# Kernel tuning notes

Measured on AMD Instinct MI355X. Metric: run time of the kernel, lower is better.

## Reference

```python
import jax, jax.numpy as jnp
import numpy as np

NC = 6  # number of classes (model=None default)
BOX_GAIN, CLS_GAIN, DFL_GAIN = 7.5, 0.5, 1.5


def setup_inputs() -> dict:
    key = jax.random.key(0)
    k0, k1, k2, kb, kc, kxy, kwh = jax.random.split(key, 7)
    bs, na, no = 32, 3, NC + 5
    pred0 = jax.random.normal(k0, (bs, na, 160, 160, no), dtype=jnp.float32)
    pred1 = jax.random.normal(k1, (bs, na, 80, 80, no), dtype=jnp.float32)
    pred2 = jax.random.normal(k2, (bs, na, 40, 40, no), dtype=jnp.float32)
    n_tgt = 8192
    b = jax.random.randint(kb, (n_tgt,), 0, bs).astype(jnp.float32)
    c = jax.random.randint(kc, (n_tgt,), 0, NC).astype(jnp.float32)
    xy = jax.random.uniform(kxy, (n_tgt, 2), minval=0.02, maxval=0.98)
    wh = jax.random.uniform(kwh, (n_tgt, 2), minval=0.02, maxval=0.3)
    targets = jnp.concatenate([b[:, None], c[:, None], xy, wh], axis=1)  # [N,6]
    return {"pred0": pred0, "pred1": pred1, "pred2": pred2, "targets": targets}


def _layer_loss(pred, b, c, txywh):
    # pred: [bs, na, ny, nx, no]; matches: per-target gather at anchor 0
    bs, na, ny, nx, no = pred.shape
    n = txywh.shape[0]
    # int(nx*tx) truncation; coords positive so floor == trunc
    gx = jnp.clip(jnp.floor(nx * txywh[:, 0]).astype(jnp.int32), 0, nx - 1)
    gy = jnp.clip(jnp.floor(ny * txywh[:, 1]).astype(jnp.int32), 0, ny - 1)
    p = pred[b, 0, gy, gx]  # [N, no] gathered predictions
    lbox = jnp.abs(p[:, :4] - txywh).sum()                 # L1, reduction='sum'
    lobj = jax.nn.softplus(-p[:, 4]).sum()                 # BCE-with-logits vs 1
    p_cls = p[:, 5:5 + NC]                                  # [N, NC]
    t_cls = jax.nn.one_hot(c, NC, dtype=p_cls.dtype)
    lcls = (jax.nn.softplus(p_cls) - p_cls * t_cls).sum()  # BCE-with-logits vs one-hot
    inv_n = 1.0 / jnp.maximum(1, n)
    return lbox * inv_n, lobj * inv_n, lcls * inv_n


def reference(pred0, pred1, pred2, targets):
    b = targets[:, 0].astype(jnp.int32)
    c = targets[:, 1].astype(jnp.int32)
    txywh = targets[:, 2:6]
    lbox = jnp.zeros((), jnp.float32)
    lobj = jnp.zeros((), jnp.float32)
    lcls = jnp.zeros((), jnp.float32)
    for pred in (pred0, pred1, pred2):
        db, do, dc = _layer_loss(pred, b, c, txywh)
        lbox, lobj, lcls = lbox + db, lobj + do, lcls + dc
    # NOTE: source multiplies lobj by dfl_gain (reproduced faithfully)
    lbox = lbox * BOX_GAIN
    lobj = lobj * DFL_GAIN
    lcls = lcls * CLS_GAIN
    loss = lbox + lobj + lcls
    return loss, lbox, lobj, lcls
```

## Files before the change

kernel.cpp:

```cpp
#include <hip/hip_runtime.h>

#define NCLS 6
#define NO 11
#define TAG 0x5D3C0DEu

__device__ __forceinline__ float softplusf(float x) {
    return log1pf(expf(-fabsf(x))) + fmaxf(x, 0.0f);
}

__global__ void __launch_bounds__(256) detloss_fused(
        const float* __restrict__ pred0,
        const float* __restrict__ pred1,
        const float* __restrict__ pred2,
        const float* __restrict__ targets,
        unsigned long long* __restrict__ slots,
        float* __restrict__ out,
        int n_tgt, int nwaves, float inv_n) {
    const int stride = gridDim.x * blockDim.x;
    float lbox = 0.0f, lobj = 0.0f, lcls = 0.0f;
    for (int i = blockIdx.x * blockDim.x + threadIdx.x; i < n_tgt; i += stride) {
        const float2* t2 = (const float2*)(targets + (size_t)i * 6);
        const float2 q0 = t2[0], q1 = t2[1], q2 = t2[2];
        const int   b  = (int)q0.x;
        const int   c  = (int)q0.y;
        const float tx = q1.x, ty = q1.y, tw = q2.x, th = q2.y;
        const float* preds[3] = {pred0, pred1, pred2};
        const int    dims[3]  = {160, 80, 40};
        #pragma unroll
        for (int l = 0; l < 3; ++l) {
            const int nx = dims[l], ny = dims[l];
            int gx = (int)floorf((float)nx * tx); gx = min(max(gx, 0), nx - 1);
            int gy = (int)floorf((float)ny * ty); gy = min(max(gy, 0), ny - 1);
            const float* p = preds[l] +
                ((size_t)b * 3u * (size_t)ny * (size_t)nx +
                 (size_t)gy * (size_t)nx + (size_t)gx) * NO;
            lbox += fabsf(p[0] - tx) + fabsf(p[1] - ty) +
                    fabsf(p[2] - tw) + fabsf(p[3] - th);
            lobj += softplusf(-p[4]);
            float prod = 1.0f;
            #pragma unroll
            for (int j = 0; j < NCLS; ++j) prod *= (1.0f + expf(p[5 + j]));
            lcls += logf(prod) - p[5 + c];
        }
    }

    #pragma unroll
    for (int off = 32; off > 0; off >>= 1) {
        lbox += __shfl_down(lbox, off);
        lobj += __shfl_down(lobj, off);
        lcls += __shfl_down(lcls, off);
    }
    const int wid  = threadIdx.x >> 6;
    const int lane = threadIdx.x & 63;
    const int wglobal = blockIdx.x * (blockDim.x >> 6) + wid;
    if (lane == 0) {
        const int s0 = wglobal * 3;
        atomicExch(&slots[s0 + 0], ((unsigned long long)TAG << 32) | __float_as_uint(lbox));
        atomicExch(&slots[s0 + 1], ((unsigned long long)TAG << 32) | __float_as_uint(lobj));
        atomicExch(&slots[s0 + 2], ((unsigned long long)TAG << 32) | __float_as_uint(lcls));
    }
    if (blockIdx.x != 0) return;

    __shared__ float sP[3][128];
    __shared__ float sR[3];
    const int tid    = threadIdx.x;
    const int nslots = nwaves * 3;
    if (tid < nslots) {
        unsigned long long w;
        do { w = atomicAdd(&slots[tid], 0ull); } while ((unsigned)(w >> 32) != TAG);
        atomicExch(&slots[tid], 0ull);
        sP[tid % 3][tid / 3] = __uint_as_float((unsigned)w);
    }
    if (tid + 256 < nslots) {
        const int s = tid + 256;
        unsigned long long w;
        do { w = atomicAdd(&slots[s], 0ull); } while ((unsigned)(w >> 32) != TAG);
        atomicExch(&slots[s], 0ull);
        sP[s % 3][s / 3] = __uint_as_float((unsigned)w);
    }
    __syncthreads();

    if (wid < 3) {
        float v = sP[wid][lane] + sP[wid][lane + 64];
        #pragma unroll
        for (int off = 32; off > 0; off >>= 1) v += __shfl_down(v, off);
        if (lane == 0) sR[wid] = v;
    }
    __syncthreads();

    if (tid == 0) {
        const float LB = sR[0] * inv_n * 7.5f;
        const float LO = sR[1] * inv_n * 1.5f;
        const float LC = sR[2] * inv_n * 0.5f;
        out[0] = LB + LO + LC;
        out[1] = LB;
        out[2] = LO;
        out[3] = LC;
    }
}

extern "C" void kernel_launch(void* const* d_in, const int* in_sizes, int n_in,
                              void* d_out, int out_size, void* d_ws, size_t ws_size,
                              hipStream_t stream) {
    const float* pred0   = (const float*)d_in[0];
    const float* pred1   = (const float*)d_in[1];
    const float* pred2   = (const float*)d_in[2];
    const float* targets = (const float*)d_in[3];
    float* out = (float*)d_out;
    unsigned long long* slots = (unsigned long long*)d_ws;

    const int n_tgt = in_sizes[3] / 6;
    const float inv_n = 1.0f / (float)(n_tgt > 0 ? n_tgt : 1);

    const int block = 256;
    int grid = (n_tgt + block - 1) / block;
    if (grid > 32) grid = 32;
    const int nwaves = grid * (block / 64);

    detloss_fused<<<grid, block, 0, stream>>>(pred0, pred1, pred2, targets,
                                              slots, out, n_tgt, nwaves, inv_n);
}
```

Measured before the change: 9.974 us.

## Dedicate block zero to reduction and replace RMW atomics with relaxed loads/stores

Adds a separate consumer block that only gathers the per-wave partial sums, so the producer blocks no longer include one that also spins. Replaces atomicAdd-polling and atomicExch with relaxed agent-scope atomic loads and stores. Folds the per-target softplus and log calls into running products with a single log at the end, which removes transcendental work but risks overflow or underflow of the product over many targets per thread.

```diff
diff --git a/kernel.cpp b/kernel.cpp
--- a/kernel.cpp
+++ b/kernel.cpp
@@ -3,10 +3,6 @@
 #define NCLS 6
 #define NO 11
 #define TAG 0x5D3C0DEu
-
-__device__ __forceinline__ float softplusf(float x) {
-    return log1pf(expf(-fabsf(x))) + fmaxf(x, 0.0f);
-}
 
 __global__ void __launch_bounds__(256) detloss_fused(
         const float* __restrict__ pred0,
@@ -16,69 +12,88 @@
         unsigned long long* __restrict__ slots,
         float* __restrict__ out,
         int n_tgt, int nwaves, float inv_n) {
-    const int stride = gridDim.x * blockDim.x;
-    float lbox = 0.0f, lobj = 0.0f, lcls = 0.0f;
-    for (int i = blockIdx.x * blockDim.x + threadIdx.x; i < n_tgt; i += stride) {
-        const float2* t2 = (const float2*)(targets + (size_t)i * 6);
-        const float2 q0 = t2[0], q1 = t2[1], q2 = t2[2];
-        const int   b  = (int)q0.x;
-        const int   c  = (int)q0.y;
-        const float tx = q1.x, ty = q1.y, tw = q2.x, th = q2.y;
-        const float* preds[3] = {pred0, pred1, pred2};
-        const int    dims[3]  = {160, 80, 40};
+    const int tid  = threadIdx.x;
+    const int wid  = tid >> 6;
+    const int lane = tid & 63;
+
+    if (blockIdx.x != 0) {
+        const int nprod  = gridDim.x - 1;
+        const int stride = nprod * blockDim.x;
+        float lbox = 0.0f, prod_obj = 1.0f, prod_cls = 1.0f, sub = 0.0f;
+        for (int i = (blockIdx.x - 1) * blockDim.x + tid; i < n_tgt; i += stride) {
+            const float2* t2 = (const float2*)(targets + (size_t)i * 6);
+            const float2 q0 = t2[0], q1 = t2[1], q2 = t2[2];
+            const int   b  = (int)q0.x;
+            const int   c  = (int)q0.y;
+            const float tx = q1.x, ty = q1.y, tw = q2.x, th = q2.y;
+            const float* preds[3] = {pred0, pred1, pred2};
+            const int    dims[3]  = {160, 80, 40};
+            #pragma unroll
+            for (int l = 0; l < 3; ++l) {
+                const int nx = dims[l], ny = dims[l];
+                int gx = (int)floorf((float)nx * tx); gx = min(max(gx, 0), nx - 1);
+                int gy = (int)floorf((float)ny * ty); gy = min(max(gy, 0), ny - 1);
+                const float* p = preds[l] +
+                    ((size_t)b * 3u * (size_t)ny * (size_t)nx +
+                     (size_t)gy * (size_t)nx + (size_t)gx) * NO;
+                lbox += fabsf(p[0] - tx) + fabsf(p[1] - ty) +
+                        fabsf(p[2] - tw) + fabsf(p[3] - th);
+                prod_obj *= 1.0f + expf(-p[4]);
+                #pragma unroll
+                for (int j = 0; j < NCLS; ++j) prod_cls *= 1.0f + expf(p[5 + j]);
+                sub += p[5 + c];
+            }
+        }
+        float lobj = logf(prod_obj);
+        float lcls = logf(prod_cls) - sub;
+
         #pragma unroll
-        for (int l = 0; l < 3; ++l) {
-            const int nx = dims[l], ny = dims[l];
-            int gx = (int)floorf((float)nx * tx); gx = min(max(gx, 0), nx - 1);
-            int gy = (int)floorf((float)ny * ty); gy = min(max(gy, 0), ny - 1);
-            const float* p = preds[l] +
-                ((size_t)b * 3u * (size_t)ny * (size_t)nx +
-                 (size_t)gy * (size_t)nx + (size_t)gx) * NO;
-            lbox += fabsf(p[0] - tx) + fabsf(p[1] - ty) +
-                    fabsf(p[2] - tw) + fabsf(p[3] - th);
-            lobj += softplusf(-p[4]);
-            float prod = 1.0f;
-            #pragma unroll
-            for (int j = 0; j < NCLS; ++j) prod *= (1.0f + expf(p[5 + j]));
-            lcls += logf(prod) - p[5 + c];
+        for (int off = 32; off > 0; off >>= 1) {
+            lbox += __shfl_down(lbox, off);
+            lobj += __shfl_down(lobj, off);
+            lcls += __shfl_down(lcls, off);
         }
+        if (lane == 0) {
+            const int s0 = ((blockIdx.x - 1) * (blockDim.x >> 6) + wid) * 3;
+            __hip_atomic_store(&slots[s0 + 0],
+                ((unsigned long long)TAG << 32) | __float_as_uint(lbox),
+                __ATOMIC_RELAXED, __HIP_MEMORY_SCOPE_AGENT);
+            __hip_atomic_store(&slots[s0 + 1],
+                ((unsigned long long)TAG << 32) | __float_as_uint(lobj),
+                __ATOMIC_RELAXED, __HIP_MEMORY_SCOPE_AGENT);
+            __hip_atomic_store(&slots[s0 + 2],
+                ((unsigned long long)TAG << 32) | __float_as_uint(lcls),
+                __ATOMIC_RELAXED, __HIP_MEMORY_SCOPE_AGENT);
+        }
+        return;
     }
-
-    #pragma unroll
-    for (int off = 32; off > 0; off >>= 1) {
-        lbox += __shfl_down(lbox, off);
-        lobj += __shfl_down(lobj, off);
-        lcls += __shfl_down(lcls, off);
-    }
-    const int wid  = threadIdx.x >> 6;
-    const int lane = threadIdx.x & 63;
-    const int wglobal = blockIdx.x * (blockDim.x >> 6) + wid;
-    if (lane == 0) {
-        const int s0 = wglobal * 3;
-        atomicExch(&slots[s0 + 0], ((unsigned long long)TAG << 32) | __float_as_uint(lbox));
-        atomicExch(&slots[s0 + 1], ((unsigned long long)TAG << 32) | __float_as_uint(lobj));
-        atomicExch(&slots[s0 + 2], ((unsigned long long)TAG << 32) | __float_as_uint(lcls));
-    }
-    if (blockIdx.x != 0) return;
 
     __shared__ float sP[3][128];
     __shared__ float sR[3];
-    const int tid    = threadIdx.x;
     const int nslots = nwaves * 3;
-    if (tid < nslots) {
+    const bool has1 = (tid < nslots);
+    const bool has2 = (tid + 256 < nslots);
+    if (has1) {
         unsigned long long w;
-        do { w = atomicAdd(&slots[tid], 0ull); } while ((unsigned)(w >> 32) != TAG);
-        atomicExch(&slots[tid], 0ull);
+        do { w = __hip_atomic_load(&slots[tid], __ATOMIC_RELAXED,
+                                   __HIP_MEMORY_SCOPE_AGENT); }
+        while ((unsigned)(w >> 32) != TAG);
         sP[tid % 3][tid / 3] = __uint_as_float((unsigned)w);
     }
-    if (tid + 256 < nslots) {
+    if (has2) {
         const int s = tid + 256;
         unsigned long long w;
-        do { w = atomicAdd(&slots[s], 0ull); } while ((unsigned)(w >> 32) != TAG);
-        atomicExch(&slots[s], 0ull);
+        do { w = __hip_atomic_load(&slots[s], __ATOMIC_RELAXED,
+                                   __HIP_MEMORY_SCOPE_AGENT); }
+        while ((unsigned)(w >> 32) != TAG);
         sP[s % 3][s / 3] = __uint_as_float((unsigned)w);
     }
     __syncthreads();
+
+    if (has1) __hip_atomic_store(&slots[tid], 0ull, __ATOMIC_RELAXED,
+                                 __HIP_MEMORY_SCOPE_AGENT);
+    if (has2) __hip_atomic_store(&slots[tid + 256], 0ull, __ATOMIC_RELAXED,
+                                 __HIP_MEMORY_SCOPE_AGENT);
 
     if (wid < 3) {
         float v = sP[wid][lane] + sP[wid][lane + 64];
@@ -113,10 +128,10 @@
     const float inv_n = 1.0f / (float)(n_tgt > 0 ? n_tgt : 1);
 
     const int block = 256;
-    int grid = (n_tgt + block - 1) / block;
-    if (grid > 32) grid = 32;
-    const int nwaves = grid * (block / 64);
+    int nprod = (n_tgt + block - 1) / block;
+    if (nprod > 32) nprod = 32;
+    const int nwaves = nprod * (block / 64);
 
-    detloss_fused<<<grid, block, 0, stream>>>(pred0, pred1, pred2, targets,
-                                              slots, out, n_tgt, nwaves, inv_n);
+    detloss_fused<<<nprod + 1, block, 0, stream>>>(pred0, pred1, pred2, targets,
+                                                   slots, out, n_tgt, nwaves, inv_n);
 }
```

Result: faster. 9.736 us (-2.4%).
